# Optimization experiments

Measured on AMD Instinct MI355X. Metric: run time of the kernel, lower is better.

The kernel has to match this reference:

```python
import jax, jax.numpy as jnp
import numpy as np

N = 100000
M = 1600000
IN_C = 64
OUT_C = 64


def setup_inputs() -> dict:
    key = jax.random.key(0)
    k1, k2, k3 = jax.random.split(key, 3)
    x = jax.random.normal(k1, (N, IN_C), dtype=jnp.float32)
    edge_index = jax.random.randint(k2, (2, M), 0, N, dtype=jnp.int64)
    # glorot-initialized linear weight (no bias in lin)
    limit = np.sqrt(6.0 / (IN_C + OUT_C))
    W = jax.random.uniform(k3, (IN_C, OUT_C), dtype=jnp.float32, minval=-limit, maxval=limit)
    b = jnp.zeros((OUT_C,), dtype=jnp.float32)  # zeros() init for bias
    return {"x": x, "edge_index": edge_index, "W": W, "b": b}


def reference(x, edge_index, W, b):
    # x: [N, in_c] -> lin -> [N, out_c]
    h = x @ W
    n = x.shape[0]
    row, col = edge_index[0], edge_index[1]  # source, target

    # add self loops (fill_value = 1.0 since improved=False)
    loop = jnp.arange(n, dtype=edge_index.dtype)
    row = jnp.concatenate([row, loop])
    col = jnp.concatenate([col, loop])
    w = jnp.ones(row.shape[0], dtype=h.dtype)  # edge_weight defaults to ones

    # symmetric gcn normalization: deg over target nodes
    deg = jax.ops.segment_sum(w, col, num_segments=n)
    deg_inv_sqrt = deg ** -0.5
    deg_inv_sqrt = jnp.where(jnp.isinf(deg_inv_sqrt), 0.0, deg_inv_sqrt)
    norm = deg_inv_sqrt[row] * w * deg_inv_sqrt[col]  # [M+N]

    # spmm: aggregate normalized source messages at targets
    msgs = norm[:, None] * h[row]  # [M+N, out_c]
    out = jax.ops.segment_sum(msgs, col, num_segments=n)  # [N, out_c]
    return out + b
```

## Files before the change

kernel.cpp:

```cpp
#include <hip/hip_runtime.h>

#define N_NODES 100000
#define M_EDGES 1600000
#define CH 64
#define NPB 128
#define NB ((N_NODES + NPB - 1) / NPB)
#define PART_CHUNK 8192
#define PART_BLOCKS ((M_EDGES + PART_CHUNK - 1) / PART_CHUNK)
#define REG_E 12
#define GROWS 192
#define GBLKS ((N_NODES + GROWS - 1) / GROWS)

__device__ __forceinline__ unsigned int pack_bf16x2(float a, float b) {
    unsigned int ua = __float_as_uint(a);
    ua = (ua + 0x7fffu + ((ua >> 16) & 1u)) >> 16;
    unsigned int ub = __float_as_uint(b);
    ub = (ub + 0x7fffu + ((ub >> 16) & 1u)) >> 16;
    return ua | (ub << 16);
}
__device__ __forceinline__ float bf_lo(unsigned int u) { return __uint_as_float(u << 16); }
__device__ __forceinline__ float bf_hi(unsigned int u) { return __uint_as_float(u & 0xffff0000u); }

__global__ __launch_bounds__(256) void k_bhist(const int* __restrict__ col, int* __restrict__ T) {
    __shared__ int h[NB];
    int tid = threadIdx.x;
    for (int i = tid; i < NB; i += 256) h[i] = 0;
    __syncthreads();
    const int4* c4 = (const int4*)col;
    int start4 = blockIdx.x * (PART_CHUNK / 4);
    int end4 = min(M_EDGES / 4, start4 + PART_CHUNK / 4);
    for (int e = start4 + tid; e < end4; e += 256) {
        int4 v = c4[e];
        atomicAdd(&h[v.x >> 7], 1);
        atomicAdd(&h[v.y >> 7], 1);
        atomicAdd(&h[v.z >> 7], 1);
        atomicAdd(&h[v.w >> 7], 1);
    }
    __syncthreads();
    for (int i = tid; i < NB; i += 256) T[blockIdx.x * NB + i] = h[i];
}

__global__ __launch_bounds__(256) void k_colsum(int* __restrict__ T, int* __restrict__ tot) {
    __shared__ int s[256];
    int b = blockIdx.x, t = threadIdx.x;
    int v = (t < PART_BLOCKS) ? T[t * NB + b] : 0;
    s[t] = v;
    __syncthreads();
    for (int off = 1; off < 256; off <<= 1) {
        int tv = (t >= off) ? s[t - off] : 0;
        __syncthreads();
        s[t] += tv;
        __syncthreads();
    }
    if (t < PART_BLOCKS) T[t * NB + b] = s[t] - v;
    if (t == 255) tot[b] = s[255];
}

__global__ __launch_bounds__(1024) void k_bucket_scan(const int* __restrict__ tot, int* __restrict__ bbase) {
    __shared__ int s[1024];
    int t = threadIdx.x;
    int v = (t < NB) ? tot[t] : 0;
    s[t] = v;
    __syncthreads();
    for (int off = 1; off < 1024; off <<= 1) {
        int tv = (t >= off) ? s[t - off] : 0;
        __syncthreads();
        s[t] += tv;
        __syncthreads();
    }
    if (t < NB) bbase[t] = s[t] - v;
    if (t == NB - 1) bbase[NB] = s[t];
}

__global__ __launch_bounds__(256) void k_partition(const int* __restrict__ row, const int* __restrict__ col,
                                                   const int* __restrict__ bbase, const int* __restrict__ T,
                                                   unsigned int* __restrict__ pairs) {
    __shared__ int h[NB];
    int tid = threadIdx.x;
    int c = blockIdx.x;
    for (int i = tid; i < NB; i += 256) h[i] = bbase[i] + T[c * NB + i];
    __syncthreads();
    const int4* c4 = (const int4*)col;
    const int4* r4 = (const int4*)row;
    int start4 = c * (PART_CHUNK / 4);
    int end4 = min(M_EDGES / 4, start4 + PART_CHUNK / 4);
    for (int e = start4 + tid; e < end4; e += 256) {
        int4 cc = c4[e];
        int4 rr = r4[e];
        int pos;
        pos = atomicAdd(&h[cc.x >> 7], 1);
        pairs[pos] = ((unsigned int)rr.x << 7) | (unsigned int)(cc.x & 127);
        pos = atomicAdd(&h[cc.y >> 7], 1);
        pairs[pos] = ((unsigned int)rr.y << 7) | (unsigned int)(cc.y & 127);
        pos = atomicAdd(&h[cc.z >> 7], 1);
        pairs[pos] = ((unsigned int)rr.z << 7) | (unsigned int)(cc.z & 127);
        pos = atomicAdd(&h[cc.w >> 7], 1);
        pairs[pos] = ((unsigned int)rr.w << 7) | (unsigned int)(cc.w & 127);
    }
}

__global__ __launch_bounds__(256) void k_fine(const int* __restrict__ bbase,
                                              unsigned int* __restrict__ pairs, int* __restrict__ node_start,
                                              float* __restrict__ dis) {
    __shared__ int lcnt[NPB];
    __shared__ int lcur[NPB];
    __shared__ int ss[NPB];
    int b = blockIdx.x, t = threadIdx.x;
    int s0 = bbase[b], e0 = bbase[b + 1];

    if (t < NPB) lcnt[t] = 0;
    __syncthreads();

    unsigned int reg[REG_E];
#pragma unroll
    for (int k = 0; k < REG_E; k++) {
        int e = s0 + t + k * 256;
        if (e < e0) {
            unsigned int p = pairs[e];
            reg[k] = p;
            atomicAdd(&lcnt[p & 127u], 1);
        }
    }
    __syncthreads();

    int v = 0;
    if (t < NPB) { v = lcnt[t]; ss[t] = v; }
    __syncthreads();
    for (int off = 1; off < NPB; off <<= 1) {
        int tv = (t < NPB && t >= off) ? ss[t - off] : 0;
        __syncthreads();
        if (t < NPB) ss[t] += tv;
        __syncthreads();
    }
    if (t < NPB) {
        int excl = ss[t] - v;
        lcur[t] = excl;
        int node = b * NPB + t;
        if (node < N_NODES) {
            node_start[node] = s0 + excl;
            dis[node] = 1.0f / sqrtf((float)(v + 1));
        }
        if (b == NB - 1 && t == 0) node_start[N_NODES] = e0;
    }
    __syncthreads();

#pragma unroll
    for (int k = 0; k < REG_E; k++) {
        int e = s0 + t + k * 256;
        if (e < e0) {
            unsigned int p = reg[k];
            int pos = atomicAdd(&lcur[p & 127u], 1);
            pairs[s0 + pos] = p >> 7;
        }
    }
}

__global__ __launch_bounds__(256) void k_gemm_g(const float* __restrict__ x, const float* __restrict__ W,
                                                const float* __restrict__ dis, unsigned int* __restrict__ g2) {
    __shared__ float sW[64][64];
    __shared__ float sXf[GROWS * 65];
    int t = threadIdx.x;
    int row0 = blockIdx.x * GROWS;
    int nrows = min(GROWS, N_NODES - row0);

    for (int i = t; i < 64 * 64; i += 256) sW[i >> 6][i & 63] = W[i];
    const float4* xv = (const float4*)x;
    for (int idx = t; idx < GROWS * 16; idx += 256) {
        int r = idx >> 4, c4 = idx & 15;
        float4 v = (r < nrows) ? xv[(size_t)(row0 + r) * 16 + c4] : make_float4(0.f, 0.f, 0.f, 0.f);
        sXf[r * 65 + c4 * 4 + 0] = v.x;
        sXf[r * 65 + c4 * 4 + 1] = v.y;
        sXf[r * 65 + c4 * 4 + 2] = v.z;
        sXf[r * 65 + c4 * 4 + 3] = v.w;
    }
    __syncthreads();

    int q = t >> 6;
    int rid = t & 63;
    int c0 = q * 16;
    float acc0[16], acc1[16], acc2[16];
#pragma unroll
    for (int j = 0; j < 16; j++) { acc0[j] = 0.f; acc1[j] = 0.f; acc2[j] = 0.f; }

    for (int k = 0; k < 64; k++) {
        float xv0 = sXf[rid * 65 + k];
        float xv1 = sXf[(rid + 64) * 65 + k];
        float xv2 = sXf[(rid + 128) * 65 + k];
        const float4* wp = (const float4*)&sW[k][c0];
        float4 w0 = wp[0], w1 = wp[1], w2 = wp[2], w3 = wp[3];
        float wv[16] = {w0.x, w0.y, w0.z, w0.w, w1.x, w1.y, w1.z, w1.w,
                        w2.x, w2.y, w2.z, w2.w, w3.x, w3.y, w3.z, w3.w};
#pragma unroll
        for (int j = 0; j < 16; j++) {
            acc0[j] += xv0 * wv[j];
            acc1[j] += xv1 * wv[j];
            acc2[j] += xv2 * wv[j];
        }
    }

#pragma unroll
    for (int jr = 0; jr < 3; jr++) {
        int r = rid + jr * 64;
        int gr = row0 + r;
        if (r < nrows) {
            float* accp = (jr == 0) ? acc0 : (jr == 1) ? acc1 : acc2;
            float d = dis[gr];
            uint4 wlo, whi;
            wlo.x = pack_bf16x2(d * accp[0], d * accp[1]);
            wlo.y = pack_bf16x2(d * accp[2], d * accp[3]);
            wlo.z = pack_bf16x2(d * accp[4], d * accp[5]);
            wlo.w = pack_bf16x2(d * accp[6], d * accp[7]);
            whi.x = pack_bf16x2(d * accp[8], d * accp[9]);
            whi.y = pack_bf16x2(d * accp[10], d * accp[11]);
            whi.z = pack_bf16x2(d * accp[12], d * accp[13]);
            whi.w = pack_bf16x2(d * accp[14], d * accp[15]);
            unsigned int base = (unsigned int)gr * 32 + q * 8;
            *reinterpret_cast<uint4*>(&g2[base]) = wlo;
            *reinterpret_cast<uint4*>(&g2[base + 4]) = whi;
        }
    }
}

__global__ __launch_bounds__(256) void k_aggregate(const int* __restrict__ nstart, const int* __restrict__ srow,
                                                   const float* __restrict__ dis, const unsigned int* __restrict__ g2,
                                                   const float* __restrict__ bias, float* __restrict__ out) {
    int node = blockIdx.x * 8 + (threadIdx.x >> 5);
    if (node >= N_NODES) return;
    int l = threadIdx.x & 31;
    int grp = l >> 3;
    int sub = l & 7;
    const uint4* gq = (const uint4*)g2;
    int s0 = nstart[node];
    int e0 = nstart[node + 1];
    float a0 = 0.f, a1 = 0.f, a2 = 0.f, a3 = 0.f, a4 = 0.f, a5 = 0.f, a6 = 0.f, a7 = 0.f;
    int e0m1 = e0 - 1;
    for (int i = s0; i < e0; i += 16) {
        int ea = i + grp, eb = i + 4 + grp, ec = i + 8 + grp, ed = i + 12 + grp;
        int r0 = srow[min(ea, e0m1)];
        int r1 = srow[min(eb, e0m1)];
        int r2 = srow[min(ec, e0m1)];
        int r3 = srow[min(ed, e0m1)];
        uint4 u0 = gq[(unsigned int)r0 * 8 + sub];
        uint4 u1 = gq[(unsigned int)r1 * 8 + sub];
        uint4 u2 = gq[(unsigned int)r2 * 8 + sub];
        uint4 u3 = gq[(unsigned int)r3 * 8 + sub];
        if (ea < e0) { a0 += bf_lo(u0.x); a1 += bf_hi(u0.x); a2 += bf_lo(u0.y); a3 += bf_hi(u0.y);
                       a4 += bf_lo(u0.z); a5 += bf_hi(u0.z); a6 += bf_lo(u0.w); a7 += bf_hi(u0.w); }
        if (eb < e0) { a0 += bf_lo(u1.x); a1 += bf_hi(u1.x); a2 += bf_lo(u1.y); a3 += bf_hi(u1.y);
                       a4 += bf_lo(u1.z); a5 += bf_hi(u1.z); a6 += bf_lo(u1.w); a7 += bf_hi(u1.w); }
        if (ec < e0) { a0 += bf_lo(u2.x); a1 += bf_hi(u2.x); a2 += bf_lo(u2.y); a3 += bf_hi(u2.y);
                       a4 += bf_lo(u2.z); a5 += bf_hi(u2.z); a6 += bf_lo(u2.w); a7 += bf_hi(u2.w); }
        if (ed < e0) { a0 += bf_lo(u3.x); a1 += bf_hi(u3.x); a2 += bf_lo(u3.y); a3 += bf_hi(u3.y);
                       a4 += bf_lo(u3.z); a5 += bf_hi(u3.z); a6 += bf_lo(u3.w); a7 += bf_hi(u3.w); }
    }
    a0 += __shfl_xor(a0, 8, 64); a0 += __shfl_xor(a0, 16, 64);
    a1 += __shfl_xor(a1, 8, 64); a1 += __shfl_xor(a1, 16, 64);
    a2 += __shfl_xor(a2, 8, 64); a2 += __shfl_xor(a2, 16, 64);
    a3 += __shfl_xor(a3, 8, 64); a3 += __shfl_xor(a3, 16, 64);
    a4 += __shfl_xor(a4, 8, 64); a4 += __shfl_xor(a4, 16, 64);
    a5 += __shfl_xor(a5, 8, 64); a5 += __shfl_xor(a5, 16, 64);
    a6 += __shfl_xor(a6, 8, 64); a6 += __shfl_xor(a6, 16, 64);
    a7 += __shfl_xor(a7, 8, 64); a7 += __shfl_xor(a7, 16, 64);
    if (grp == 0) {
        uint4 su = gq[(unsigned int)node * 8 + sub];
        a0 += bf_lo(su.x); a1 += bf_hi(su.x); a2 += bf_lo(su.y); a3 += bf_hi(su.y);
        a4 += bf_lo(su.z); a5 += bf_hi(su.z); a6 += bf_lo(su.w); a7 += bf_hi(su.w);
        float d = dis[node];
        const float4* b4 = (const float4*)bias;
        float4 bv0 = b4[2 * sub], bv1 = b4[2 * sub + 1];
        float4* o4 = (float4*)&out[(size_t)node * CH + 8 * sub];
        o4[0] = make_float4(d * a0 + bv0.x, d * a1 + bv0.y, d * a2 + bv0.z, d * a3 + bv0.w);
        o4[1] = make_float4(d * a4 + bv1.x, d * a5 + bv1.y, d * a6 + bv1.z, d * a7 + bv1.w);
    }
}

extern "C" void kernel_launch(void* const* d_in, const int* in_sizes, int n_in,
                              void* d_out, int out_size, void* d_ws, size_t ws_size,
                              hipStream_t stream) {
    const float* x  = (const float*)d_in[0];
    const int*   ei = (const int*)d_in[1];
    const float* W  = (const float*)d_in[2];
    const float* bv = (const float*)d_in[3];
    float* out = (float*)d_out;

    const int* row = ei;
    const int* col = ei + M_EDGES;

    char* ws = (char*)d_ws;
    int*          tot   = (int*)(ws + 0);
    int*          bbase = (int*)(ws + (4 << 10));
    float*        dis   = (float*)(ws + (512 << 10));
    int*          nstart= (int*)(ws + (1024 << 10));
    int*          T     = (int*)(ws + (1536 << 10));
    unsigned int* g2    = (unsigned int*)(ws + (3u << 20));
    unsigned int* pairs = (unsigned int*)(ws + (16u << 20));

    k_bhist<<<PART_BLOCKS, 256, 0, stream>>>(col, T);
    k_colsum<<<NB, 256, 0, stream>>>(T, tot);
    k_bucket_scan<<<1, 1024, 0, stream>>>(tot, bbase);
    k_partition<<<PART_BLOCKS, 256, 0, stream>>>(row, col, bbase, T, pairs);
    k_fine<<<NB, 256, 0, stream>>>(bbase, pairs, nstart, dis);
    k_gemm_g<<<GBLKS, 256, 0, stream>>>(x, W, dis, g2);
    k_aggregate<<<(N_NODES + 7) / 8, 256, 0, stream>>>(nstart, (const int*)pairs, dis, g2, bv, out);
}
```

Before: 184.4 us.

## Merge bucket count scan into one kernel, use atomic bucket offsets, unroll aggregate

Replaces the per-bucket column-sum kernel and the separate bucket scan with a single 1024-thread kernel that sums each bucket's counts across partition blocks and scans them. The partition kernel now claims each block's offset within a bucket with a global atomicAdd on a cursor array instead of reading precomputed exclusive prefixes, which removes one launch. Within a bucket, edge order now depends on nondeterministic atomic ordering. The aggregate loop is also unrolled to 8 gathers per group per iteration, and the self-loop and degree loads are hoisted above the loop to raise memory-level parallelism. The single-block sum is serial over 196 rows and uses more registers in aggregate.

```diff
diff --git a/kernel.cpp b/kernel.cpp
--- a/kernel.cpp
+++ b/kernel.cpp
@@ -40,27 +40,16 @@
     for (int i = tid; i < NB; i += 256) T[blockIdx.x * NB + i] = h[i];
 }
 
-__global__ __launch_bounds__(256) void k_colsum(int* __restrict__ T, int* __restrict__ tot) {
-    __shared__ int s[256];
-    int b = blockIdx.x, t = threadIdx.x;
-    int v = (t < PART_BLOCKS) ? T[t * NB + b] : 0;
-    s[t] = v;
-    __syncthreads();
-    for (int off = 1; off < 256; off <<= 1) {
-        int tv = (t >= off) ? s[t - off] : 0;
-        __syncthreads();
-        s[t] += tv;
-        __syncthreads();
-    }
-    if (t < PART_BLOCKS) T[t * NB + b] = s[t] - v;
-    if (t == 255) tot[b] = s[255];
-}
-
-__global__ __launch_bounds__(1024) void k_bucket_scan(const int* __restrict__ tot, int* __restrict__ bbase) {
+__global__ __launch_bounds__(1024) void k_sumscan(const int* __restrict__ T, int* __restrict__ bbase,
+                                                  int* __restrict__ bcur) {
     __shared__ int s[1024];
     int t = threadIdx.x;
-    int v = (t < NB) ? tot[t] : 0;
-    s[t] = v;
+    int sum = 0;
+    if (t < NB) {
+#pragma unroll 4
+        for (int c = 0; c < PART_BLOCKS; c++) sum += T[c * NB + t];
+    }
+    s[t] = sum;
     __syncthreads();
     for (int off = 1; off < 1024; off <<= 1) {
         int tv = (t >= off) ? s[t - off] : 0;
@@ -68,17 +57,24 @@
         s[t] += tv;
         __syncthreads();
     }
-    if (t < NB) bbase[t] = s[t] - v;
+    if (t < NB) {
+        int e = s[t] - sum;
+        bbase[t] = e;
+        bcur[t] = e;
+    }
     if (t == NB - 1) bbase[NB] = s[t];
 }
 
 __global__ __launch_bounds__(256) void k_partition(const int* __restrict__ row, const int* __restrict__ col,
-                                                   const int* __restrict__ bbase, const int* __restrict__ T,
+                                                   int* __restrict__ bcur, const int* __restrict__ T,
                                                    unsigned int* __restrict__ pairs) {
     __shared__ int h[NB];
     int tid = threadIdx.x;
     int c = blockIdx.x;
-    for (int i = tid; i < NB; i += 256) h[i] = bbase[i] + T[c * NB + i];
+    for (int i = tid; i < NB; i += 256) {
+        int cnt = T[c * NB + i];
+        h[i] = cnt ? atomicAdd(&bcur[i], cnt) : 0;
+    }
     __syncthreads();
     const int4* c4 = (const int4*)col;
     const int4* r4 = (const int4*)row;
@@ -232,26 +228,45 @@
     const uint4* gq = (const uint4*)g2;
     int s0 = nstart[node];
     int e0 = nstart[node + 1];
+    uint4 su = gq[(unsigned int)node * 8 + sub];
+    float d = dis[node];
     float a0 = 0.f, a1 = 0.f, a2 = 0.f, a3 = 0.f, a4 = 0.f, a5 = 0.f, a6 = 0.f, a7 = 0.f;
     int e0m1 = e0 - 1;
-    for (int i = s0; i < e0; i += 16) {
-        int ea = i + grp, eb = i + 4 + grp, ec = i + 8 + grp, ed = i + 12 + grp;
-        int r0 = srow[min(ea, e0m1)];
-        int r1 = srow[min(eb, e0m1)];
-        int r2 = srow[min(ec, e0m1)];
-        int r3 = srow[min(ed, e0m1)];
+    for (int i = s0; i < e0; i += 32) {
+        int ea0 = i + grp,      ea1 = i + 4 + grp,  ea2 = i + 8 + grp,  ea3 = i + 12 + grp;
+        int ea4 = i + 16 + grp, ea5 = i + 20 + grp, ea6 = i + 24 + grp, ea7 = i + 28 + grp;
+        int r0 = srow[min(ea0, e0m1)];
+        int r1 = srow[min(ea1, e0m1)];
+        int r2 = srow[min(ea2, e0m1)];
+        int r3 = srow[min(ea3, e0m1)];
+        int r4 = srow[min(ea4, e0m1)];
+        int r5 = srow[min(ea5, e0m1)];
+        int r6 = srow[min(ea6, e0m1)];
+        int r7 = srow[min(ea7, e0m1)];
         uint4 u0 = gq[(unsigned int)r0 * 8 + sub];
         uint4 u1 = gq[(unsigned int)r1 * 8 + sub];
         uint4 u2 = gq[(unsigned int)r2 * 8 + sub];
         uint4 u3 = gq[(unsigned int)r3 * 8 + sub];
-        if (ea < e0) { a0 += bf_lo(u0.x); a1 += bf_hi(u0.x); a2 += bf_lo(u0.y); a3 += bf_hi(u0.y);
-                       a4 += bf_lo(u0.z); a5 += bf_hi(u0.z); a6 += bf_lo(u0.w); a7 += bf_hi(u0.w); }
-        if (eb < e0) { a0 += bf_lo(u1.x); a1 += bf_hi(u1.x); a2 += bf_lo(u1.y); a3 += bf_hi(u1.y);
-                       a4 += bf_lo(u1.z); a5 += bf_hi(u1.z); a6 += bf_lo(u1.w); a7 += bf_hi(u1.w); }
-        if (ec < e0) { a0 += bf_lo(u2.x); a1 += bf_hi(u2.x); a2 += bf_lo(u2.y); a3 += bf_hi(u2.y);
-                       a4 += bf_lo(u2.z); a5 += bf_hi(u2.z); a6 += bf_lo(u2.w); a7 += bf_hi(u2.w); }
-        if (ed < e0) { a0 += bf_lo(u3.x); a1 += bf_hi(u3.x); a2 += bf_lo(u3.y); a3 += bf_hi(u3.y);
-                       a4 += bf_lo(u3.z); a5 += bf_hi(u3.z); a6 += bf_lo(u3.w); a7 += bf_hi(u3.w); }
+        uint4 u4 = gq[(unsigned int)r4 * 8 + sub];
+        uint4 u5 = gq[(unsigned int)r5 * 8 + sub];
+        uint4 u6 = gq[(unsigned int)r6 * 8 + sub];
+        uint4 u7 = gq[(unsigned int)r7 * 8 + sub];
+        if (ea0 < e0) { a0 += bf_lo(u0.x); a1 += bf_hi(u0.x); a2 += bf_lo(u0.y); a3 += bf_hi(u0.y);
+                        a4 += bf_lo(u0.z); a5 += bf_hi(u0.z); a6 += bf_lo(u0.w); a7 += bf_hi(u0.w); }
+        if (ea1 < e0) { a0 += bf_lo(u1.x); a1 += bf_hi(u1.x); a2 += bf_lo(u1.y); a3 += bf_hi(u1.y);
+                        a4 += bf_lo(u1.z); a5 += bf_hi(u1.z); a6 += bf_lo(u1.w); a7 += bf_hi(u1.w); }
+        if (ea2 < e0) { a0 += bf_lo(u2.x); a1 += bf_hi(u2.x); a2 += bf_lo(u2.y); a3 += bf_hi(u2.y);
+                        a4 += bf_lo(u2.z); a5 += bf_hi(u2.z); a6 += bf_lo(u2.w); a7 += bf_hi(u2.w); }
+        if (ea3 < e0) { a0 += bf_lo(u3.x); a1 += bf_hi(u3.x); a2 += bf_lo(u3.y); a3 += bf_hi(u3.y);
+                        a4 += bf_lo(u3.z); a5 += bf_hi(u3.z); a6 += bf_lo(u3.w); a7 += bf_hi(u3.w); }
+        if (ea4 < e0) { a0 += bf_lo(u4.x); a1 += bf_hi(u4.x); a2 += bf_lo(u4.y); a3 += bf_hi(u4.y);
+                        a4 += bf_lo(u4.z); a5 += bf_hi(u4.z); a6 += bf_lo(u4.w); a7 += bf_hi(u4.w); }
+        if (ea5 < e0) { a0 += bf_lo(u5.x); a1 += bf_hi(u5.x); a2 += bf_lo(u5.y); a3 += bf_hi(u5.y);
+                        a4 += bf_lo(u5.z); a5 += bf_hi(u5.z); a6 += bf_lo(u5.w); a7 += bf_hi(u5.w); }
+        if (ea6 < e0) { a0 += bf_lo(u6.x); a1 += bf_hi(u6.x); a2 += bf_lo(u6.y); a3 += bf_hi(u6.y);
+                        a4 += bf_lo(u6.z); a5 += bf_hi(u6.z); a6 += bf_lo(u6.w); a7 += bf_hi(u6.w); }
+        if (ea7 < e0) { a0 += bf_lo(u7.x); a1 += bf_hi(u7.x); a2 += bf_lo(u7.y); a3 += bf_hi(u7.y);
+                        a4 += bf_lo(u7.z); a5 += bf_hi(u7.z); a6 += bf_lo(u7.w); a7 += bf_hi(u7.w); }
     }
     a0 += __shfl_xor(a0, 8, 64); a0 += __shfl_xor(a0, 16, 64);
     a1 += __shfl_xor(a1, 8, 64); a1 += __shfl_xor(a1, 16, 64);
@@ -262,10 +277,8 @@
     a6 += __shfl_xor(a6, 8, 64); a6 += __shfl_xor(a6, 16, 64);
     a7 += __shfl_xor(a7, 8, 64); a7 += __shfl_xor(a7, 16, 64);
     if (grp == 0) {
-        uint4 su = gq[(unsigned int)node * 8 + sub];
         a0 += bf_lo(su.x); a1 += bf_hi(su.x); a2 += bf_lo(su.y); a3 += bf_hi(su.y);
         a4 += bf_lo(su.z); a5 += bf_hi(su.z); a6 += bf_lo(su.w); a7 += bf_hi(su.w);
-        float d = dis[node];
         const float4* b4 = (const float4*)bias;
         float4 bv0 = b4[2 * sub], bv1 = b4[2 * sub + 1];
         float4* o4 = (float4*)&out[(size_t)node * CH + 8 * sub];
@@ -287,8 +300,8 @@
     const int* col = ei + M_EDGES;
 
     char* ws = (char*)d_ws;
-    int*          tot   = (int*)(ws + 0);
-    int*          bbase = (int*)(ws + (4 << 10));
+    int*          bbase = (int*)(ws + 0);
+    int*          bcur  = (int*)(ws + (8 << 10));
     float*        dis   = (float*)(ws + (512 << 10));
     int*          nstart= (int*)(ws + (1024 << 10));
     int*          T     = (int*)(ws + (1536 << 10));
@@ -296,9 +309,8 @@
     unsigned int* pairs = (unsigned int*)(ws + (16u << 20));
 
     k_bhist<<<PART_BLOCKS, 256, 0, stream>>>(col, T);
-    k_colsum<<<NB, 256, 0, stream>>>(T, tot);
-    k_bucket_scan<<<1, 1024, 0, stream>>>(tot, bbase);
-    k_partition<<<PART_BLOCKS, 256, 0, stream>>>(row, col, bbase, T, pairs);
+    k_sumscan<<<1, 1024, 0, stream>>>(T, bbase, bcur);
+    k_partition<<<PART_BLOCKS, 256, 0, stream>>>(row, col, bcur, T, pairs);
     k_fine<<<NB, 256, 0, stream>>>(bbase, pairs, nstart, dis);
     k_gemm_g<<<GBLKS, 256, 0, stream>>>(x, W, dis, g2);
     k_aggregate<<<(N_NODES + 7) / 8, 256, 0, stream>>>(nstart, (const int*)pairs, dis, g2, bv, out);
```

Result: slower. 197.9 us (+7.3%).

## Replace two-pass bucket partition with fixed-capacity buckets and atomic cursors

Applied to the files above, without the earlier changes.

Drops the separate histogram, column-scan and bucket-scan kernels. Each partition block now counts its edges per bucket in shared memory and reserves space with a global atomicAdd into buckets of fixed capacity CAP. Node ranges become explicit start/end arrays so the buckets need not be contiguous. This saves launches and a full extra pass over the col array, but it assumes no bucket exceeds CAP edges and it makes the edge order nondeterministic.

```diff
diff --git a/kernel.cpp b/kernel.cpp
--- a/kernel.cpp
+++ b/kernel.cpp
@@ -5,6 +5,7 @@
 #define CH 64
 #define NPB 128
 #define NB ((N_NODES + NPB - 1) / NPB)
+#define CAP 3072
 #define PART_CHUNK 8192
 #define PART_BLOCKS ((M_EDGES + PART_CHUNK - 1) / PART_CHUNK)
 #define REG_E 12
@@ -21,13 +22,16 @@
 __device__ __forceinline__ float bf_lo(unsigned int u) { return __uint_as_float(u << 16); }
 __device__ __forceinline__ float bf_hi(unsigned int u) { return __uint_as_float(u & 0xffff0000u); }
 
-__global__ __launch_bounds__(256) void k_bhist(const int* __restrict__ col, int* __restrict__ T) {
+__global__ __launch_bounds__(256) void k_partition(const int* __restrict__ row, const int* __restrict__ col,
+                                                   int* __restrict__ bcur, unsigned int* __restrict__ pairs) {
     __shared__ int h[NB];
     int tid = threadIdx.x;
+    int c = blockIdx.x;
     for (int i = tid; i < NB; i += 256) h[i] = 0;
     __syncthreads();
     const int4* c4 = (const int4*)col;
-    int start4 = blockIdx.x * (PART_CHUNK / 4);
+    const int4* r4 = (const int4*)row;
+    int start4 = c * (PART_CHUNK / 4);
     int end4 = min(M_EDGES / 4, start4 + PART_CHUNK / 4);
     for (int e = start4 + tid; e < end4; e += 256) {
         int4 v = c4[e];
@@ -37,53 +41,11 @@
         atomicAdd(&h[v.w >> 7], 1);
     }
     __syncthreads();
-    for (int i = tid; i < NB; i += 256) T[blockIdx.x * NB + i] = h[i];
-}
-
-__global__ __launch_bounds__(256) void k_colsum(int* __restrict__ T, int* __restrict__ tot) {
-    __shared__ int s[256];
-    int b = blockIdx.x, t = threadIdx.x;
-    int v = (t < PART_BLOCKS) ? T[t * NB + b] : 0;
-    s[t] = v;
-    __syncthreads();
-    for (int off = 1; off < 256; off <<= 1) {
-        int tv = (t >= off) ? s[t - off] : 0;
-        __syncthreads();
-        s[t] += tv;
-        __syncthreads();
-    }
-    if (t < PART_BLOCKS) T[t * NB + b] = s[t] - v;
-    if (t == 255) tot[b] = s[255];
-}
-
-__global__ __launch_bounds__(1024) void k_bucket_scan(const int* __restrict__ tot, int* __restrict__ bbase) {
-    __shared__ int s[1024];
-    int t = threadIdx.x;
-    int v = (t < NB) ? tot[t] : 0;
-    s[t] = v;
-    __syncthreads();
-    for (int off = 1; off < 1024; off <<= 1) {
-        int tv = (t >= off) ? s[t - off] : 0;
-        __syncthreads();
-        s[t] += tv;
-        __syncthreads();
-    }
-    if (t < NB) bbase[t] = s[t] - v;
-    if (t == NB - 1) bbase[NB] = s[t];
-}
-
-__global__ __launch_bounds__(256) void k_partition(const int* __restrict__ row, const int* __restrict__ col,
-                                                   const int* __restrict__ bbase, const int* __restrict__ T,
-                                                   unsigned int* __restrict__ pairs) {
-    __shared__ int h[NB];
-    int tid = threadIdx.x;
-    int c = blockIdx.x;
-    for (int i = tid; i < NB; i += 256) h[i] = bbase[i] + T[c * NB + i];
-    __syncthreads();
-    const int4* c4 = (const int4*)col;
-    const int4* r4 = (const int4*)row;
-    int start4 = c * (PART_CHUNK / 4);
-    int end4 = min(M_EDGES / 4, start4 + PART_CHUNK / 4);
+    for (int i = tid; i < NB; i += 256) {
+        int cnt = h[i];
+        h[i] = cnt ? (i * CAP + atomicAdd(&bcur[i], cnt)) : 0;
+    }
+    __syncthreads();
     for (int e = start4 + tid; e < end4; e += 256) {
         int4 cc = c4[e];
         int4 rr = r4[e];
@@ -99,14 +61,15 @@
     }
 }
 
-__global__ __launch_bounds__(256) void k_fine(const int* __restrict__ bbase,
-                                              unsigned int* __restrict__ pairs, int* __restrict__ node_start,
-                                              float* __restrict__ dis) {
+__global__ __launch_bounds__(256) void k_fine(const int* __restrict__ bcur,
+                                              unsigned int* __restrict__ pairs, int* __restrict__ nstart,
+                                              int* __restrict__ nend, float* __restrict__ dis) {
     __shared__ int lcnt[NPB];
     __shared__ int lcur[NPB];
     __shared__ int ss[NPB];
     int b = blockIdx.x, t = threadIdx.x;
-    int s0 = bbase[b], e0 = bbase[b + 1];
+    int s0 = b * CAP;
+    int e0 = s0 + bcur[b];
 
     if (t < NPB) lcnt[t] = 0;
     __syncthreads();
@@ -137,10 +100,10 @@
         lcur[t] = excl;
         int node = b * NPB + t;
         if (node < N_NODES) {
-            node_start[node] = s0 + excl;
+            nstart[node] = s0 + excl;
+            nend[node] = s0 + excl + v;
             dis[node] = 1.0f / sqrtf((float)(v + 1));
         }
-        if (b == NB - 1 && t == 0) node_start[N_NODES] = e0;
     }
     __syncthreads();
 
@@ -221,8 +184,9 @@
     }
 }
 
-__global__ __launch_bounds__(256) void k_aggregate(const int* __restrict__ nstart, const int* __restrict__ srow,
-                                                   const float* __restrict__ dis, const unsigned int* __restrict__ g2,
+__global__ __launch_bounds__(256) void k_aggregate(const int* __restrict__ nstart, const int* __restrict__ nend,
+                                                   const int* __restrict__ srow, const float* __restrict__ dis,
+                                                   const unsigned int* __restrict__ g2,
                                                    const float* __restrict__ bias, float* __restrict__ out) {
     int node = blockIdx.x * 8 + (threadIdx.x >> 5);
     if (node >= N_NODES) return;
@@ -231,7 +195,7 @@
     int sub = l & 7;
     const uint4* gq = (const uint4*)g2;
     int s0 = nstart[node];
-    int e0 = nstart[node + 1];
+    int e0 = nend[node];
     float a0 = 0.f, a1 = 0.f, a2 = 0.f, a3 = 0.f, a4 = 0.f, a5 = 0.f, a6 = 0.f, a7 = 0.f;
     int e0m1 = e0 - 1;
     for (int i = s0; i < e0; i += 16) {
@@ -287,19 +251,17 @@
     const int* col = ei + M_EDGES;
 
     char* ws = (char*)d_ws;
-    int*          tot   = (int*)(ws + 0);
-    int*          bbase = (int*)(ws + (4 << 10));
+    int*          bcur  = (int*)(ws + 0);
     float*        dis   = (float*)(ws + (512 << 10));
     int*          nstart= (int*)(ws + (1024 << 10));
-    int*          T     = (int*)(ws + (1536 << 10));
+    int*          nend  = (int*)(ws + (1536 << 10));
     unsigned int* g2    = (unsigned int*)(ws + (3u << 20));
     unsigned int* pairs = (unsigned int*)(ws + (16u << 20));
 
-    k_bhist<<<PART_BLOCKS, 256, 0, stream>>>(col, T);
-    k_colsum<<<NB, 256, 0, stream>>>(T, tot);
-    k_bucket_scan<<<1, 1024, 0, stream>>>(tot, bbase);
-    k_partition<<<PART_BLOCKS, 256, 0, stream>>>(row, col, bbase, T, pairs);
-    k_fine<<<NB, 256, 0, stream>>>(bbase, pairs, nstart, dis);
+    hipMemsetAsync(bcur, 0, NB * sizeof(int), stream);
+
+    k_partition<<<PART_BLOCKS, 256, 0, stream>>>(row, col, bcur, pairs);
+    k_fine<<<NB, 256, 0, stream>>>(bcur, pairs, nstart, nend, dis);
     k_gemm_g<<<GBLKS, 256, 0, stream>>>(x, W, dis, g2);
-    k_aggregate<<<(N_NODES + 7) / 8, 256, 0, stream>>>(nstart, (const int*)pairs, dis, g2, bv, out);
-}
+    k_aggregate<<<(N_NODES + 7) / 8, 256, 0, stream>>>(nstart, nend, (const int*)pairs, dis, g2, bv, out);
+}
```

After: 180.6 us. -2.0%, faster.
